# Kernel optimization log

Hardware: AMD Instinct MI355X
Metric: run time of the kernel (lower is better)

The kernel has to match this reference:

```python
import jax, jax.numpy as jnp
import numpy as np

N_EXPERTS = 6
TOP_K = 2
AUX_COEFF = 0.01
W_SCALE = 0.02  # keep activations in a sane range with random weights


def setup_inputs() -> dict:
    key = jax.random.key(0)
    k1, k2, k3, k4 = jax.random.split(key, 4)
    B, T, D, H = 4, 2048, 1024, 4096
    x = jax.random.normal(k1, (B, T, D), dtype=jnp.float32)
    w_router = jax.random.normal(k2, (D, N_EXPERTS), dtype=jnp.float32) * W_SCALE
    w1 = jax.random.normal(k3, (N_EXPERTS, D, H), dtype=jnp.float32) * W_SCALE
    w2 = jax.random.normal(k4, (N_EXPERTS, H, D), dtype=jnp.float32) * W_SCALE
    return {"x": x, "w_router": w_router, "w1": w1, "w2": w2}


def reference(x, w_router, w1, w2):
    B, T, D = x.shape
    x_flat = x.reshape(-1, D)                              # (N, D)
    router_logits = x_flat @ w_router                      # (N, E)
    router_probs = jax.nn.softmax(router_logits, axis=-1)
    top_probs, top_idx = jax.lax.top_k(router_probs, TOP_K)  # (N, K)
    top_probs = top_probs / jnp.sum(top_probs, axis=-1, keepdims=True)
    # combine weights per (token, expert): sum over k slots hitting expert e
    onehot = jax.nn.one_hot(top_idx, N_EXPERTS, dtype=x.dtype)  # (N, K, E)
    comb = jnp.einsum('nke,nk->ne', onehot, top_probs)          # (N, E)
    out = jnp.zeros_like(x_flat)
    for e in range(N_EXPERTS):
        h = jax.nn.gelu(x_flat @ w1[e], approximate=False)      # (N, H)
        out = out + comb[:, e:e + 1] * (h @ w2[e])              # (N, D)
    tokens_per_expert = jnp.mean(router_probs, axis=0)          # (E,)
    uniform = jnp.full_like(tokens_per_expert, 1.0 / N_EXPERTS)
    aux_loss = AUX_COEFF * jnp.mean((tokens_per_expert - uniform) ** 2)
    return out.reshape(B, T, D), aux_loss
```

## Files before the change

### kernel.cpp

```cpp
#include <hip/hip_runtime.h>

#define N_TOK 8192
#define DDIM  1024
#define HDIM  4096
#define NEXP  6
#define RBLOCKS (N_TOK / 4)
#define SBLOCKS 32

typedef unsigned short ushort_t;
typedef __bf16 bf16_t;
typedef bf16_t bf16x8 __attribute__((ext_vector_type(8)));
typedef float f32x4 __attribute__((ext_vector_type(4)));

typedef const __attribute__((address_space(1))) void* gptr_t;
typedef __attribute__((address_space(3))) void* lptr_t;

__device__ __forceinline__ void g2l16(const void* g, void* l) {
    __builtin_amdgcn_global_load_lds((gptr_t)g, (lptr_t)l, 16, 0, 0);
}

__device__ __forceinline__ ushort_t f2bf(float f) {
    unsigned int u = __float_as_uint(f);
    unsigned int r = (u + 0x7FFFu + ((u >> 16) & 1u)) >> 16;
    return (ushort_t)r;
}

__global__ void convert_x_kernel(const float* __restrict__ x, ushort_t* __restrict__ xb) {
    size_t i = (size_t)(blockIdx.x * 256 + threadIdx.x) * 8;
    float4 a = *(const float4*)(x + i);
    float4 b = *(const float4*)(x + i + 4);
    union { ushort_t u[8]; uint4 v; } o;
    o.u[0] = f2bf(a.x); o.u[1] = f2bf(a.y); o.u[2] = f2bf(a.z); o.u[3] = f2bf(a.w);
    o.u[4] = f2bf(b.x); o.u[5] = f2bf(b.y); o.u[6] = f2bf(b.z); o.u[7] = f2bf(b.w);
    *(uint4*)(xb + i) = o.v;
}

__global__ void transpose_bf16_kernel(const float* __restrict__ src, ushort_t* __restrict__ dst,
                                      int R, int C) {
    __shared__ float tile[32][33];
    size_t msz = (size_t)R * C;
    src += (size_t)blockIdx.z * msz;
    dst += (size_t)blockIdx.z * msz;
    int c0 = blockIdx.x * 32, r0 = blockIdx.y * 32;
    int tx = threadIdx.x & 31, ty = threadIdx.x >> 5;
#pragma unroll
    for (int i = 0; i < 4; ++i)
        tile[ty + 8 * i][tx] = src[(size_t)(r0 + ty + 8 * i) * C + c0 + tx];
    __syncthreads();
#pragma unroll
    for (int i = 0; i < 4; ++i)
        dst[(size_t)(c0 + ty + 8 * i) * R + r0 + tx] = f2bf(tile[tx][ty + 8 * i]);
}

__global__ void router_kernel(const float* __restrict__ x, const float* __restrict__ wr,
                              int* __restrict__ tok_e, float* __restrict__ tok_w,
                              float* __restrict__ part_p, int* __restrict__ part_c) {
    __shared__ float bsum[NEXP];
    __shared__ int bcnt[NEXP];
    int wid = threadIdx.x >> 6, l = threadIdx.x & 63;
    if (threadIdx.x < NEXP) { bsum[threadIdx.x] = 0.f; bcnt[threadIdx.x] = 0; }
    __syncthreads();
    int t = blockIdx.x * 4 + wid;
    const float* xr = x + (size_t)t * DDIM;
    float acc[NEXP] = {0.f, 0.f, 0.f, 0.f, 0.f, 0.f};
#pragma unroll
    for (int c = 0; c < 4; ++c) {
        int k0 = c * 256 + l * 4;
        float4 xv = *(const float4*)(xr + k0);
        float wv[24];
#pragma unroll
        for (int q = 0; q < 6; ++q)
            *(float4*)(wv + 4 * q) = *(const float4*)(wr + (size_t)k0 * NEXP + 4 * q);
        float xa[4] = {xv.x, xv.y, xv.z, xv.w};
#pragma unroll
        for (int r = 0; r < 4; ++r)
#pragma unroll
            for (int e = 0; e < NEXP; ++e) acc[e] += xa[r] * wv[r * NEXP + e];
    }
#pragma unroll
    for (int e = 0; e < NEXP; ++e)
#pragma unroll
        for (int d = 32; d >= 1; d >>= 1) acc[e] += __shfl_xor(acc[e], d);
    if (l == 0) {
        float m = acc[0];
#pragma unroll
        for (int e = 1; e < NEXP; ++e) m = fmaxf(m, acc[e]);
        float p[NEXP], s = 0.f;
#pragma unroll
        for (int e = 0; e < NEXP; ++e) { p[e] = expf(acc[e] - m); s += p[e]; }
        float inv = 1.0f / s;
#pragma unroll
        for (int e = 0; e < NEXP; ++e) p[e] *= inv;
        int i1 = 0; float b1 = p[0];
#pragma unroll
        for (int e = 1; e < NEXP; ++e) if (p[e] > b1) { b1 = p[e]; i1 = e; }
        int i2 = -1; float b2 = -1.f;
#pragma unroll
        for (int e = 0; e < NEXP; ++e) if (e != i1 && p[e] > b2) { b2 = p[e]; i2 = e; }
        float swn = 1.0f / (b1 + b2);
        tok_e[2 * t] = i1; tok_e[2 * t + 1] = i2;
        tok_w[2 * t] = b1 * swn; tok_w[2 * t + 1] = b2 * swn;
        atomicAdd(&bcnt[i1], 1);
        atomicAdd(&bcnt[i2], 1);
#pragma unroll
        for (int e = 0; e < NEXP; ++e) atomicAdd(&bsum[e], p[e]);
    }
    __syncthreads();
    if (threadIdx.x < NEXP) {
        part_p[(size_t)blockIdx.x * NEXP + threadIdx.x] = bsum[threadIdx.x];
        part_c[(size_t)blockIdx.x * NEXP + threadIdx.x] = bcnt[threadIdx.x];
    }
}

__global__ void finalize_kernel(const float* __restrict__ part_p, const int* __restrict__ part_c,
                                int* __restrict__ counts, int* __restrict__ offs,
                                float* __restrict__ aux_out) {
    __shared__ float redp[NEXP][4];
    __shared__ int redc[NEXP][4];
    int tid = threadIdx.x, wid = tid >> 6, l = tid & 63;
    float myp[NEXP] = {0.f, 0.f, 0.f, 0.f, 0.f, 0.f};
    int myc[NEXP] = {0, 0, 0, 0, 0, 0};
    for (int b = tid; b < RBLOCKS; b += 256) {
#pragma unroll
        for (int e = 0; e < NEXP; ++e) {
            myp[e] += part_p[(size_t)b * NEXP + e];
            myc[e] += part_c[(size_t)b * NEXP + e];
        }
    }
#pragma unroll
    for (int e = 0; e < NEXP; ++e) {
#pragma unroll
        for (int d = 32; d >= 1; d >>= 1) {
            myp[e] += __shfl_xor(myp[e], d);
            myc[e] += __shfl_xor(myc[e], d);
        }
        if (l == 0) { redp[e][wid] = myp[e]; redc[e][wid] = myc[e]; }
    }
    __syncthreads();
    if (tid == 0) {
        int o = 0;
        float s = 0.f;
        for (int e = 0; e < NEXP; ++e) {
            int c = redc[e][0] + redc[e][1] + redc[e][2] + redc[e][3];
            float ps = redp[e][0] + redp[e][1] + redp[e][2] + redp[e][3];
            counts[e] = c;
            offs[e] = o;
            o += c;
            float d = ps / (float)N_TOK - (1.0f / 6.0f);
            s += d * d;
        }
        offs[NEXP] = o;
        aux_out[0] = 0.01f * (s / 6.0f);
    }
}

__global__ void scatter_kernel(const int* __restrict__ tok_e, const float* __restrict__ tok_w,
                               const int* __restrict__ offs, int* __restrict__ cursors,
                               int* __restrict__ slot_token, float* __restrict__ slot_w) {
    __shared__ int lcnt[NEXP], lbase[NEXP];
    int tid = threadIdx.x;
    if (tid < NEXP) lcnt[tid] = 0;
    __syncthreads();
    int t = blockIdx.x * 256 + tid;
    int e0 = tok_e[2 * t], e1 = tok_e[2 * t + 1];
    int r0 = atomicAdd(&lcnt[e0], 1);
    int r1 = atomicAdd(&lcnt[e1], 1);
    __syncthreads();
    if (tid < NEXP) lbase[tid] = atomicAdd(&cursors[tid], lcnt[tid]);
    __syncthreads();
    int i0 = offs[e0] + lbase[e0] + r0;
    slot_token[i0] = t; slot_w[i0] = tok_w[2 * t];
    int i1 = offs[e1] + lbase[e1] + r1;
    slot_token[i1] = t; slot_w[i1] = tok_w[2 * t + 1];
}

template <int LAYER>
__global__ __launch_bounds__(256, 2)
void moe_gemm_kernel(const ushort_t* __restrict__ A, const ushort_t* __restrict__ Bt,
                     ushort_t* __restrict__ Hout, float* __restrict__ Out,
                     const int* __restrict__ slot_token, const float* __restrict__ slot_w,
                     const int* __restrict__ offs, const int* __restrict__ counts) {
    constexpr int Kd = (LAYER == 1) ? DDIM : HDIM;
    constexpr int Nd = (LAYER == 1) ? HDIM : DDIM;
    const int e = blockIdx.z;
    const int cnt = counts[e];
    const int mbase = blockIdx.y * 128;
    if (mbase >= cnt) return;
    const int nbase = blockIdx.x * 128;
    const int off = offs[e];
    const ushort_t* Bte = Bt + (size_t)e * ((size_t)Nd * Kd);

    __shared__ __align__(16) ushort_t lds[8192];

    const int tid = threadIdx.x;
    const int wid = tid >> 6, l = tid & 63;

    size_t aoff[2], boff[2];
#pragma unroll
    for (int j = 0; j < 2; ++j) {
        int row = (j * 256 + tid) >> 2;
        int slot = tid & 3;
        int kg = slot ^ ((row >> 1) & 3);
        int lr = mbase + row;
        int lrc = lr < cnt - 1 ? lr : cnt - 1;
        size_t arow;
        if (LAYER == 1) arow = (size_t)slot_token[off + lrc] * DDIM;
        else            arow = (size_t)(off + lrc) * HDIM;
        aoff[j] = arow + (size_t)kg * 8;
        boff[j] = (size_t)(nbase + row) * Kd + (size_t)kg * 8;
    }
    ushort_t* ldsA0 = lds + wid * 512;
    ushort_t* ldsA1 = lds + 2048 + wid * 512;
    ushort_t* ldsB0 = lds + 4096 + wid * 512;
    ushort_t* ldsB1 = lds + 6144 + wid * 512;

    const int lm = l & 15, kg = l >> 4;
    const char* ldsAb = (const char*)lds;
    const char* ldsBb = (const char*)(lds + 4096);
    const int wm = (wid & 1) * 64, wn = (wid >> 1) * 64;
    int arowb[4], browb[4];
#pragma unroll
    for (int f = 0; f < 4; ++f) {
        int ar = wm + f * 16 + lm;
        arowb[f] = ar * 64 + ((kg ^ ((ar >> 1) & 3)) << 4);
        int br = wn + f * 16 + lm;
        browb[f] = br * 64 + ((kg ^ ((br >> 1) & 3)) << 4);
    }

    f32x4 acc[4][4] = {};

    for (int kt = 0; kt < Kd; kt += 32) {
        g2l16(A + aoff[0] + kt, ldsA0);
        g2l16(A + aoff[1] + kt, ldsA1);
        g2l16(Bte + boff[0] + kt, ldsB0);
        g2l16(Bte + boff[1] + kt, ldsB1);
        __syncthreads();
        bf16x8 af[4], bfv[4];
#pragma unroll
        for (int f = 0; f < 4; ++f) {
            af[f]  = *(const bf16x8*)(ldsAb + arowb[f]);
            bfv[f] = *(const bf16x8*)(ldsBb + browb[f]);
        }
#pragma unroll
        for (int i = 0; i < 4; ++i)
#pragma unroll
            for (int jj = 0; jj < 4; ++jj)
                acc[i][jj] = __builtin_amdgcn_mfma_f32_16x16x32_bf16(af[i], bfv[jj], acc[i][jj], 0, 0, 0);
        __syncthreads();
    }

    if (LAYER == 1) {
#pragma unroll
        for (int i = 0; i < 4; ++i) {
#pragma unroll
            for (int r = 0; r < 4; ++r) {
                int row = wm + i * 16 + kg * 4 + r;
                int grow = mbase + row;
                if (grow < cnt) {
                    size_t hbase = (size_t)(off + grow) * HDIM + nbase + wn + lm;
#pragma unroll
                    for (int jj = 0; jj < 4; ++jj) {
                        float v = acc[i][jj][r];
                        float g = 0.5f * v * (1.0f + erff(v * 0.70710678118654752f));
                        Hout[hbase + jj * 16] = f2bf(g);
                    }
                }
            }
        }
    } else {
#pragma unroll
        for (int i = 0; i < 4; ++i) {
#pragma unroll
            for (int r = 0; r < 4; ++r) {
                int row = wm + i * 16 + kg * 4 + r;
                int grow = mbase + row;
                if (grow < cnt) {
                    int si = off + grow;
                    int tok = slot_token[si];
                    float wgt = slot_w[si];
                    float* obase = Out + (size_t)tok * DDIM + nbase + wn + lm;
#pragma unroll
                    for (int jj = 0; jj < 4; ++jj)
                        atomicAdd(obase + jj * 16, wgt * acc[i][jj][r]);
                }
            }
        }
    }
}

extern "C" void kernel_launch(void* const* d_in, const int* in_sizes, int n_in,
                              void* d_out, int out_size, void* d_ws, size_t ws_size,
                              hipStream_t stream) {
    const float* x  = (const float*)d_in[0];
    const float* wr = (const float*)d_in[1];
    const float* w1 = (const float*)d_in[2];
    const float* w2 = (const float*)d_in[3];
    float* out = (float*)d_out;

    char* ws = (char*)d_ws;
    size_t o = 0;
    ushort_t* xb   = (ushort_t*)(ws + o); o += (size_t)N_TOK * DDIM * 2;
    ushort_t* w1t  = (ushort_t*)(ws + o); o += (size_t)NEXP * HDIM * DDIM * 2;
    ushort_t* w2t  = (ushort_t*)(ws + o); o += (size_t)NEXP * DDIM * HDIM * 2;
    ushort_t* hbuf = (ushort_t*)(ws + o); o += (size_t)2 * N_TOK * HDIM * 2;
    int*   tok_e   = (int*)(ws + o);   o += (size_t)N_TOK * 2 * 4;
    float* tok_w   = (float*)(ws + o); o += (size_t)N_TOK * 2 * 4;
    int*   slot_token = (int*)(ws + o);   o += (size_t)2 * N_TOK * 4;
    float* slot_w     = (float*)(ws + o); o += (size_t)2 * N_TOK * 4;
    float* part_p  = (float*)(ws + o); o += (size_t)RBLOCKS * NEXP * 4;
    int*   part_c  = (int*)(ws + o);   o += (size_t)RBLOCKS * NEXP * 4;
    int*   counts  = (int*)(ws + o);   o += 32;
    int*   cursors = (int*)(ws + o);   o += 32;
    int*   offs    = (int*)(ws + o);   o += 32;

    hipMemsetAsync(d_out, 0, (size_t)out_size * sizeof(float), stream);
    hipMemsetAsync(cursors, 0, 32, stream);

    convert_x_kernel<<<dim3(N_TOK * DDIM / 8 / 256), 256, 0, stream>>>(x, xb);
    transpose_bf16_kernel<<<dim3(HDIM / 32, DDIM / 32, NEXP), 256, 0, stream>>>(w1, w1t, DDIM, HDIM);
    transpose_bf16_kernel<<<dim3(DDIM / 32, HDIM / 32, NEXP), 256, 0, stream>>>(w2, w2t, HDIM, DDIM);
    router_kernel<<<dim3(RBLOCKS), 256, 0, stream>>>(x, wr, tok_e, tok_w, part_p, part_c);
    finalize_kernel<<<dim3(1), 256, 0, stream>>>(part_p, part_c, counts, offs, out + (size_t)N_TOK * DDIM);
    scatter_kernel<<<dim3(SBLOCKS), 256, 0, stream>>>(tok_e, tok_w, offs, cursors, slot_token, slot_w);
    moe_gemm_kernel<1><<<dim3(HDIM / 128, N_TOK / 128, NEXP), 256, 0, stream>>>(
        xb, w1t, hbuf, nullptr, slot_token, slot_w, offs, counts);
    moe_gemm_kernel<2><<<dim3(DDIM / 128, N_TOK / 128, NEXP), 256, 0, stream>>>(
        hbuf, w2t, nullptr, out, slot_token, slot_w, offs, counts);
}
```

Baseline: 567.5 us.

## Rewrite MoE GEMMs as 256x256 tile 8-wave pipelined kernels with split-K

```diff
diff --git a/kernel.cpp b/kernel.cpp
--- a/kernel.cpp
+++ b/kernel.cpp
@@ -174,114 +174,167 @@
     slot_token[i1] = t; slot_w[i1] = tok_w[2 * t + 1];
 }
 
-template <int LAYER>
-__global__ __launch_bounds__(256, 2)
-void moe_gemm_kernel(const ushort_t* __restrict__ A, const ushort_t* __restrict__ Bt,
-                     ushort_t* __restrict__ Hout, float* __restrict__ Out,
-                     const int* __restrict__ slot_token, const float* __restrict__ slot_w,
-                     const int* __restrict__ offs, const int* __restrict__ counts) {
+
+#define STAGE_A(SIG, H, KT) do { \
+    g2l16(srcA[H][0] + (KT) * 64, sA + (SIG) * 32768 + (H) * 16384 + dst0); \
+    g2l16(srcA[H][1] + (KT) * 64, sA + (SIG) * 32768 + (H) * 16384 + dst1); \
+  } while (0)
+
+#define STAGE_B(SIG, H, KT) do { \
+    g2l16(srcB[H][0] + (KT) * 64, sB + (SIG) * 32768 + (H) * 16384 + dst0); \
+    g2l16(srcB[H][1] + (KT) * 64, sB + (SIG) * 32768 + (H) * 16384 + dst1); \
+  } while (0)
+
+#define PH(SIG, Q, STG, Q3) do { \
+    bf16x8 aa[2][2]; \
+    if ((Q) == 0) { \
+      _Pragma("unroll") for (int n = 0; n < 4; ++n) \
+        _Pragma("unroll") for (int s = 0; s < 2; ++s) \
+          bb[n][s] = *(const bf16x8*)(sB + (SIG) * 32768 + bBase[s] + n * 2048); \
+    } \
+    _Pragma("unroll") for (int mi = 0; mi < 2; ++mi) \
+      _Pragma("unroll") for (int s = 0; s < 2; ++s) \
+        aa[mi][s] = *(const bf16x8*)(sA + (SIG) * 32768 + aBase[s] + ((Q) * 2 + mi) * 2048); \
+    STG; \
+    __builtin_amdgcn_s_barrier(); \
+    asm volatile("s_waitcnt lgkmcnt(0)" ::: "memory"); \
+    __builtin_amdgcn_sched_barrier(0); \
+    __builtin_amdgcn_s_setprio(1); \
+    _Pragma("unroll") for (int mi = 0; mi < 2; ++mi) \
+      _Pragma("unroll") for (int n = 0; n < 4; ++n) \
+        _Pragma("unroll") for (int s = 0; s < 2; ++s) \
+          acc[(Q) * 2 + mi][n] = __builtin_amdgcn_mfma_f32_16x16x32_bf16(aa[mi][s], bb[n][s], acc[(Q) * 2 + mi][n], 0, 0, 0); \
+    __builtin_amdgcn_s_setprio(0); \
+    if (Q3) { asm volatile("s_waitcnt vmcnt(4)" ::: "memory"); __builtin_amdgcn_sched_barrier(0); } \
+    __builtin_amdgcn_s_barrier(); \
+  } while (0)
+
+template <int LAYER, int SK>
+__global__ __launch_bounds__(512, 2)
+void moe_gemm8(const ushort_t* __restrict__ A, const ushort_t* __restrict__ Bt,
+               ushort_t* __restrict__ Hout, float* __restrict__ Out,
+               const int* __restrict__ slot_token, const float* __restrict__ slot_w,
+               const int* __restrict__ offs, const int* __restrict__ counts) {
     constexpr int Kd = (LAYER == 1) ? DDIM : HDIM;
     constexpr int Nd = (LAYER == 1) ? HDIM : DDIM;
-    const int e = blockIdx.z;
+    constexpr int KLOC = Kd / SK;
+    constexpr int NT = KLOC / 64;
+    constexpr int NX = Nd / 256;
+    extern __shared__ char smem[];
+
+    const int z = blockIdx.z;
+    const int e = z / SK, ks = z % SK;
     const int cnt = counts[e];
-    const int mbase = blockIdx.y * 128;
+    const int nwg = NX * gridDim.y;
+    int L = blockIdx.x + NX * blockIdx.y;
+    int q8 = nwg >> 3, r8 = nwg & 7;
+    int xcd = L & 7, lo = L >> 3;
+    int wg = (xcd < r8 ? xcd * (q8 + 1) : r8 * (q8 + 1) + (xcd - r8) * q8) + lo;
+    const int nbase = (wg % NX) * 256;
+    const int mbase = (wg / NX) * 256;
     if (mbase >= cnt) return;
-    const int nbase = blockIdx.x * 128;
     const int off = offs[e];
-    const ushort_t* Bte = Bt + (size_t)e * ((size_t)Nd * Kd);
-
-    __shared__ __align__(16) ushort_t lds[8192];
+    const ushort_t* Be = Bt + (size_t)e * ((size_t)Nd * Kd);
+    const int kbase = ks * KLOC;
 
     const int tid = threadIdx.x;
     const int wid = tid >> 6, l = tid & 63;
 
-    size_t aoff[2], boff[2];
-#pragma unroll
-    for (int j = 0; j < 2; ++j) {
-        int row = (j * 256 + tid) >> 2;
-        int slot = tid & 3;
-        int kg = slot ^ ((row >> 1) & 3);
-        int lr = mbase + row;
-        int lrc = lr < cnt - 1 ? lr : cnt - 1;
-        size_t arow;
-        if (LAYER == 1) arow = (size_t)slot_token[off + lrc] * DDIM;
-        else            arow = (size_t)(off + lrc) * HDIM;
-        aoff[j] = arow + (size_t)kg * 8;
-        boff[j] = (size_t)(nbase + row) * Kd + (size_t)kg * 8;
-    }
-    ushort_t* ldsA0 = lds + wid * 512;
-    ushort_t* ldsA1 = lds + 2048 + wid * 512;
-    ushort_t* ldsB0 = lds + 4096 + wid * 512;
-    ushort_t* ldsB1 = lds + 6144 + wid * 512;
+    const ushort_t* srcA[2][2];
+    const ushort_t* srcB[2][2];
+    int dst0, dst1;
+    {
+        int p0 = wid * 128 + l, p1 = wid * 128 + 64 + l;
+        dst0 = p0 * 16; dst1 = p1 * 16;
+#pragma unroll
+        for (int j = 0; j < 2; ++j) {
+            int p = j ? p1 : p0;
+            int row = p >> 3;
+            int cs = (p & 7) ^ (row & 7);
+#pragma unroll
+            for (int h = 0; h < 2; ++h) {
+                int gr = mbase + h * 128 + row;
+                int grc = gr < cnt - 1 ? gr : cnt - 1;
+                size_t arow;
+                if (LAYER == 1) arow = (size_t)slot_token[off + grc] * DDIM;
+                else            arow = (size_t)(off + grc) * HDIM;
+                srcA[h][j] = A + arow + kbase + cs * 8;
+                srcB[h][j] = Be + (size_t)(nbase + h * 128 + row) * Kd + kbase + cs * 8;
+            }
+        }
+    }
+    char* sA = smem;
+    char* sB = smem + 65536;
 
     const int lm = l & 15, kg = l >> 4;
-    const char* ldsAb = (const char*)lds;
-    const char* ldsBb = (const char*)(lds + 4096);
-    const int wm = (wid & 1) * 64, wn = (wid >> 1) * 64;
-    int arowb[4], browb[4];
-#pragma unroll
-    for (int f = 0; f < 4; ++f) {
-        int ar = wm + f * 16 + lm;
-        arowb[f] = ar * 64 + ((kg ^ ((ar >> 1) & 3)) << 4);
-        int br = wn + f * 16 + lm;
-        browb[f] = br * 64 + ((kg ^ ((br >> 1) & 3)) << 4);
-    }
-
-    f32x4 acc[4][4] = {};
-
-    for (int kt = 0; kt < Kd; kt += 32) {
-        g2l16(A + aoff[0] + kt, ldsA0);
-        g2l16(A + aoff[1] + kt, ldsA1);
-        g2l16(Bte + boff[0] + kt, ldsB0);
-        g2l16(Bte + boff[1] + kt, ldsB1);
-        __syncthreads();
-        bf16x8 af[4], bfv[4];
-#pragma unroll
-        for (int f = 0; f < 4; ++f) {
-            af[f]  = *(const bf16x8*)(ldsAb + arowb[f]);
-            bfv[f] = *(const bf16x8*)(ldsBb + browb[f]);
-        }
-#pragma unroll
-        for (int i = 0; i < 4; ++i)
-#pragma unroll
-            for (int jj = 0; jj < 4; ++jj)
-                acc[i][jj] = __builtin_amdgcn_mfma_f32_16x16x32_bf16(af[i], bfv[jj], acc[i][jj], 0, 0, 0);
-        __syncthreads();
-    }
+    const int wr = wid & 1, wc = wid >> 1;
+    const int rowA = wr * 128 + lm;
+    const int rowB = wc * 64 + lm;
+    int aBase[2], bBase[2];
+#pragma unroll
+    for (int s = 0; s < 2; ++s) {
+        aBase[s] = rowA * 128 + ((s * 4 + kg) ^ (rowA & 7)) * 16;
+        bBase[s] = rowB * 128 + ((s * 4 + kg) ^ (rowB & 7)) * 16;
+    }
+
+    f32x4 acc[8][4] = {};
+    bf16x8 bb[4][2];
+
+    STAGE_B(0, 0, 0); STAGE_B(0, 1, 0);
+    STAGE_A(0, 0, 0); STAGE_A(0, 1, 0);
+    STAGE_B(1, 0, 1); STAGE_B(1, 1, 1);
+    asm volatile("s_waitcnt vmcnt(4)" ::: "memory");
+    __builtin_amdgcn_sched_barrier(0);
+    __builtin_amdgcn_s_barrier();
+
+    for (int it = 0; it < NT / 2; ++it) {
+        const int T1 = 2 * it + 1;
+        const int F = (2 * it + 2 < NT) ? 2 * it + 2 : NT - 1;
+        const int G = (2 * it + 3 < NT) ? 2 * it + 3 : NT - 1;
+        PH(0, 0, STAGE_A(1, 0, T1), 0);
+        PH(0, 1, STAGE_A(1, 1, T1), 0);
+        PH(0, 2, STAGE_B(0, 0, F), 0);
+        PH(0, 3, STAGE_B(0, 1, F), 1);
+        PH(1, 0, STAGE_A(0, 0, F), 0);
+        PH(1, 1, STAGE_A(0, 1, F), 0);
+        PH(1, 2, STAGE_B(1, 0, G), 0);
+        PH(1, 3, STAGE_B(1, 1, G), 1);
+    }
+    asm volatile("s_waitcnt vmcnt(0)" ::: "memory");
+    __builtin_amdgcn_s_barrier();
 
     if (LAYER == 1) {
 #pragma unroll
-        for (int i = 0; i < 4; ++i) {
-#pragma unroll
-            for (int r = 0; r < 4; ++r) {
-                int row = wm + i * 16 + kg * 4 + r;
-                int grow = mbase + row;
+        for (int fm = 0; fm < 8; ++fm) {
+#pragma unroll
+            for (int rr = 0; rr < 4; ++rr) {
+                int grow = mbase + wr * 128 + fm * 16 + kg * 4 + rr;
                 if (grow < cnt) {
-                    size_t hbase = (size_t)(off + grow) * HDIM + nbase + wn + lm;
-#pragma unroll
-                    for (int jj = 0; jj < 4; ++jj) {
-                        float v = acc[i][jj][r];
-                        float g = 0.5f * v * (1.0f + erff(v * 0.70710678118654752f));
-                        Hout[hbase + jj * 16] = f2bf(g);
+                    size_t hbase = (size_t)(off + grow) * HDIM + nbase + wc * 64 + lm;
+#pragma unroll
+                    for (int n = 0; n < 4; ++n) {
+                        float v = acc[fm][n][rr];
+                        float u = -1.5957691216f * v * (1.0f + 0.044715f * v * v);
+                        float g = v / (1.0f + __expf(u));
+                        Hout[hbase + n * 16] = f2bf(g);
                     }
                 }
             }
         }
     } else {
 #pragma unroll
-        for (int i = 0; i < 4; ++i) {
-#pragma unroll
-            for (int r = 0; r < 4; ++r) {
-                int row = wm + i * 16 + kg * 4 + r;
-                int grow = mbase + row;
+        for (int fm = 0; fm < 8; ++fm) {
+#pragma unroll
+            for (int rr = 0; rr < 4; ++rr) {
+                int grow = mbase + wr * 128 + fm * 16 + kg * 4 + rr;
                 if (grow < cnt) {
                     int si = off + grow;
                     int tok = slot_token[si];
                     float wgt = slot_w[si];
-                    float* obase = Out + (size_t)tok * DDIM + nbase + wn + lm;
-#pragma unroll
-                    for (int jj = 0; jj < 4; ++jj)
-                        atomicAdd(obase + jj * 16, wgt * acc[i][jj][r]);
+                    float* obase = Out + (size_t)tok * DDIM + nbase + wc * 64 + lm;
+#pragma unroll
+                    for (int n = 0; n < 4; ++n)
+                        atomicAdd(obase + n * 16, wgt * acc[fm][n][rr]);
                 }
             }
         }
@@ -316,14 +369,17 @@
     hipMemsetAsync(d_out, 0, (size_t)out_size * sizeof(float), stream);
     hipMemsetAsync(cursors, 0, 32, stream);
 
+    hipFuncSetAttribute((const void*)moe_gemm8<1, 1>, hipFuncAttributeMaxDynamicSharedMemorySize, 131072);
+    hipFuncSetAttribute((const void*)moe_gemm8<2, 2>, hipFuncAttributeMaxDynamicSharedMemorySize, 131072);
+
     convert_x_kernel<<<dim3(N_TOK * DDIM / 8 / 256), 256, 0, stream>>>(x, xb);
     transpose_bf16_kernel<<<dim3(HDIM / 32, DDIM / 32, NEXP), 256, 0, stream>>>(w1, w1t, DDIM, HDIM);
     transpose_bf16_kernel<<<dim3(DDIM / 32, HDIM / 32, NEXP), 256, 0, stream>>>(w2, w2t, HDIM, DDIM);
     router_kernel<<<dim3(RBLOCKS), 256, 0, stream>>>(x, wr, tok_e, tok_w, part_p, part_c);
     finalize_kernel<<<dim3(1), 256, 0, stream>>>(part_p, part_c, counts, offs, out + (size_t)N_TOK * DDIM);
     scatter_kernel<<<dim3(SBLOCKS), 256, 0, stream>>>(tok_e, tok_w, offs, cursors, slot_token, slot_w);
-    moe_gemm_kernel<1><<<dim3(HDIM / 128, N_TOK / 128, NEXP), 256, 0, stream>>>(
+    moe_gemm8<1, 1><<<dim3(HDIM / 256, 32, NEXP), 512, 131072, stream>>>(
         xb, w1t, hbuf, nullptr, slot_token, slot_w, offs, counts);
-    moe_gemm_kernel<2><<<dim3(DDIM / 128, N_TOK / 128, NEXP), 256, 0, stream>>>(
+    moe_gemm8<2, 2><<<dim3(DDIM / 256, 32, NEXP * 2), 512, 131072, stream>>>(
         hbuf, w2t, nullptr, out, slot_token, slot_w, offs, counts);
 }
```

Result: slower. 987.5 us (+74.0%).
